# Performance work log

Measured on AMD Instinct MI355X. Metric: run time of the kernel, lower is better.

## Reference

```python
import jax, jax.numpy as jnp
import numpy as np

B, S, D, H = 4, 2048, 1024, 16
HS = D // H          # head size 64
DF = 4 * D           # ffn hidden 4096
EPS = 1e-5


def _layer_norm(x, g, b):
    mu = jnp.mean(x, axis=-1, keepdims=True)
    var = jnp.var(x, axis=-1, keepdims=True)
    return (x - mu) * jax.lax.rsqrt(var + EPS) * g + b


def setup_inputs() -> dict:
    key = jax.random.key(0)
    ks = jax.random.split(key, 12)
    s_d = 1.0 / np.sqrt(D)
    s_f = 1.0 / np.sqrt(DF)
    return {
        "x": jax.random.normal(ks[0], (B, S, D), jnp.float32),
        # per-head q/k/v projections, batched over heads: [H, D, HS]
        "wq": jax.random.uniform(ks[1], (H, D, HS), jnp.float32, -s_d, s_d),
        "wk": jax.random.uniform(ks[2], (H, D, HS), jnp.float32, -s_d, s_d),
        "wv": jax.random.uniform(ks[3], (H, D, HS), jnp.float32, -s_d, s_d),
        "proj_w": jax.random.uniform(ks[4], (D, D), jnp.float32, -s_d, s_d),
        "proj_b": jax.random.uniform(ks[5], (D,), jnp.float32, -s_d, s_d),
        "ff1_w": jax.random.uniform(ks[6], (D, DF), jnp.float32, -s_d, s_d),
        "ff1_b": jax.random.uniform(ks[7], (DF,), jnp.float32, -s_d, s_d),
        "ff2_w": jax.random.uniform(ks[8], (DF, D), jnp.float32, -s_f, s_f),
        "ff2_b": jax.random.uniform(ks[9], (D,), jnp.float32, -s_f, s_f),
        "ln1_g": jnp.ones((D,), jnp.float32),
        "ln1_b": jnp.zeros((D,), jnp.float32),
        "ln2_g": jnp.ones((D,), jnp.float32),
        "ln2_b": jnp.zeros((D,), jnp.float32),
    }


def reference(x, wq, wk, wv, proj_w, proj_b, ff1_w, ff1_b, ff2_w, ff2_b,
              ln1_g, ln1_b, ln2_g, ln2_b):
    # --- multi-head causal self-attention on ln1(x), all heads batched ---
    h = _layer_norm(x, ln1_g, ln1_b)                      # [B,S,D]
    q = jnp.einsum("bsd,hde->bhse", h, wq)                # [B,H,S,HS]
    k = jnp.einsum("bsd,hde->bhse", h, wk)
    v = jnp.einsum("bsd,hde->bhse", h, wv)
    scale = HS ** -0.5
    scores = jnp.einsum("bhse,bhte->bhst", q, k) * scale  # [B,H,S,S]
    causal = jnp.tril(jnp.ones((S, S), bool))
    scores = jnp.where(causal, scores, jnp.finfo(scores.dtype).min)
    att = jax.nn.softmax(scores, axis=-1)
    o = jnp.einsum("bhst,bhte->bhse", att, v)             # [B,H,S,HS]
    o = o.transpose(0, 2, 1, 3).reshape(B, S, D)          # concat heads
    sa = o @ proj_w + proj_b
    x = x + sa
    # --- FFN on ln2(x) ---
    h2 = _layer_norm(x, ln2_g, ln2_b)
    ff = jax.nn.relu(h2 @ ff1_w + ff1_b) @ ff2_w + ff2_b
    return x + ff
```

## Files before the change

kernel.cpp:

```cpp
#include <hip/hip_runtime.h>
#include <hip/hip_bf16.h>

#define BB 4
#define SS 2048
#define DD 1024
#define HH 16
#define HSZ 64
#define DFF 4096

typedef short short8 __attribute__((ext_vector_type(8)));
typedef float f32x4 __attribute__((ext_vector_type(4)));
typedef unsigned short us4 __attribute__((ext_vector_type(4)));

#define AS1 __attribute__((address_space(1)))
#define AS3 __attribute__((address_space(3)))

__device__ __forceinline__ unsigned short f2bf(float f) {
    return __bfloat16_as_ushort(__float2bfloat16(f));
}

__global__ __launch_bounds__(256) void pack_qkv_kernel(
    const float* __restrict__ wq, const float* __restrict__ wk,
    const float* __restrict__ wv, __hip_bfloat16* __restrict__ out)
{
    __shared__ float tile[64][65];
    const int bid = blockIdx.x;
    const int kt = bid & 15, hh = (bid >> 4) & 15, sel = bid >> 8;
    const float* src = (sel == 0) ? wq : (sel == 1) ? wk : wv;
    src += (size_t)hh * (DD * HSZ) + (size_t)kt * 64 * HSZ;
    const int tx = threadIdx.x & 63, ty = threadIdx.x >> 6;
    #pragma unroll
    for (int r = 0; r < 64; r += 4)
        tile[r + ty][tx] = src[(size_t)(r + ty) * HSZ + tx];
    __syncthreads();
    unsigned short* o = (unsigned short*)out + (size_t)(sel * DD + hh * 64) * DD + kt * 64;
    #pragma unroll
    for (int r = 0; r < 64; r += 4) {
        int e = r + ty;
        o[(size_t)e * DD + tx] = f2bf(tile[tx][e]);
    }
}

__global__ __launch_bounds__(256) void pack_T_kernel(
    const float* __restrict__ in, __hip_bfloat16* __restrict__ out, int K, int N)
{
    __shared__ float tile[64][65];
    const int nb = N >> 6;
    const int tn0 = (blockIdx.x % nb) << 6, tk0 = (blockIdx.x / nb) << 6;
    const int tx = threadIdx.x & 63, ty = threadIdx.x >> 6;
    #pragma unroll
    for (int r = 0; r < 64; r += 4)
        tile[r + ty][tx] = in[(size_t)(tk0 + r + ty) * N + tn0 + tx];
    __syncthreads();
    unsigned short* o = (unsigned short*)out;
    #pragma unroll
    for (int r = 0; r < 64; r += 4) {
        int n = r + ty;
        o[(size_t)(tn0 + n) * K + tk0 + tx] = f2bf(tile[tx][n]);
    }
}

__global__ __launch_bounds__(256) void ln_kernel(
    const float* __restrict__ x, const float* __restrict__ g,
    const float* __restrict__ b, __hip_bfloat16* __restrict__ out)
{
    int row = blockIdx.x;
    int t = threadIdx.x;
    const float4* xr = (const float4*)(x + (size_t)row * DD);
    float4 v = xr[t];
    float s = v.x + v.y + v.z + v.w;
    float ss = v.x * v.x + v.y * v.y + v.z * v.z + v.w * v.w;
    #pragma unroll
    for (int off = 32; off; off >>= 1) {
        s += __shfl_xor(s, off, 64);
        ss += __shfl_xor(ss, off, 64);
    }
    __shared__ float red[8];
    int w = t >> 6, lane = t & 63;
    if (lane == 0) { red[w] = s; red[4 + w] = ss; }
    __syncthreads();
    s = red[0] + red[1] + red[2] + red[3];
    ss = red[4] + red[5] + red[6] + red[7];
    float mu = s * (1.f / DD);
    float var = ss * (1.f / DD) - mu * mu;
    float rs = rsqrtf(var + 1e-5f);
    float4 gv = ((const float4*)g)[t];
    float4 bv = ((const float4*)b)[t];
    ushort4 pk = make_ushort4(
        f2bf((v.x - mu) * rs * gv.x + bv.x),
        f2bf((v.y - mu) * rs * gv.y + bv.y),
        f2bf((v.z - mu) * rs * gv.z + bv.z),
        f2bf((v.w - mu) * rs * gv.w + bv.w));
    *(ushort4*)((unsigned short*)out + (size_t)row * DD + t * 4) = pk;
}

template<int BN, bool BIAS, bool RELU, bool RES, bool OUTF32>
__global__ __launch_bounds__(512) void gemm_kernel(
    const __hip_bfloat16* __restrict__ A, const __hip_bfloat16* __restrict__ BT,
    const float* __restrict__ bias, const float* __restrict__ res,
    void* __restrict__ Cout, int M, int N, int K, int nbx)
{
    constexpr int NB = BN / 128;
    constexpr int NREP = BN / 64;
    __shared__ uint4 Ah[2][2][1024];
    __shared__ uint4 Bh[2][NB][1024];

    const int tid = threadIdx.x;
    const int lane = tid & 63;
    const int w = tid >> 6;
    const int lr = lane & 15, g = lane >> 4;
    const int nwg = gridDim.x;
    const int cpx = nwg >> 3;
    const int wg = blockIdx.x;
    const int swz = (wg & 7) * cpx + (wg >> 3);
    const int bx = swz % nbx, by = swz / nbx;
    const int row0 = by * 256, col0 = bx * BN;
    const int wm = w >> 2, wn = w & 3;
    const int NT = K >> 6;

    f32x4 acc0[4][NREP] = {};
    f32x4 acc1[4][NREP] = {};
    short8 bfr[NREP][2];

    auto stageA = [&](int buf, int half, int t) {
        const int k0 = t * 64;
        #pragma unroll
        for (int j = 0; j < 2; ++j) {
            int s = j * 512 + tid;
            int r = s >> 3;
            int c = (s & 7) ^ (r & 7);
            const __hip_bfloat16* src = A + (size_t)(row0 + half * 128 + r) * K + k0 + c * 8;
            __builtin_amdgcn_global_load_lds((const AS1 void*)src,
                (AS3 void*)(&Ah[buf][half][j * 512 + (tid & ~63)]), 16, 0, 0);
        }
    };
    auto stageB = [&](int buf, int half, int t) {
        const int k0 = t * 64;
        #pragma unroll
        for (int j = 0; j < 2; ++j) {
            int s = j * 512 + tid;
            int r = s >> 3;
            int c = (s & 7) ^ (r & 7);
            const __hip_bfloat16* src = BT + (size_t)(col0 + half * 128 + r) * K + k0 + c * 8;
            __builtin_amdgcn_global_load_lds((const AS1 void*)src,
                (AS3 void*)(&Bh[buf][half][j * 512 + (tid & ~63)]), 16, 0, 0);
        }
    };
    auto loadB = [&](int buf) {
        const int hb = (NB == 2) ? (wn >> 1) : 0;
        const int cb = (NB == 2) ? ((wn & 1) * 64) : (wn * 32);
        #pragma unroll
        for (int n = 0; n < NREP; ++n) {
            int c = cb + n * 16 + lr;
            #pragma unroll
            for (int kk = 0; kk < 2; ++kk)
                bfr[n][kk] = *(const short8*)&Bh[buf][hb][c * 8 + ((kk * 4 + g) ^ (c & 7))];
        }
    };
    auto phase = [&](auto& acc, int buf, int mh) {
        short8 af[4][2];
        #pragma unroll
        for (int mi = 0; mi < 4; ++mi) {
            int r = wm * 64 + mi * 16 + lr;
            #pragma unroll
            for (int kk = 0; kk < 2; ++kk)
                af[mi][kk] = *(const short8*)&Ah[buf][mh][r * 8 + ((kk * 4 + g) ^ (r & 7))];
        }
        asm volatile("s_waitcnt lgkmcnt(0)" ::: "memory");
        __builtin_amdgcn_sched_barrier(0);
        __builtin_amdgcn_s_setprio(1);
        #pragma unroll
        for (int mi = 0; mi < 4; ++mi)
            #pragma unroll
            for (int n = 0; n < NREP; ++n)
                #pragma unroll
                for (int kk = 0; kk < 2; ++kk)
                    acc[mi][n] = __builtin_amdgcn_mfma_f32_16x16x32_bf16(
                        af[mi][kk], bfr[n][kk], acc[mi][n], 0, 0, 0);
        __builtin_amdgcn_s_setprio(0);
    };

    stageA(0, 0, 0);
    stageB(0, 0, 0);
    if constexpr (NB == 2) stageB(0, 1, 0);
    stageA(0, 1, 0);
    stageA(1, 0, 1);
    if constexpr (NB == 2) stageB(1, 0, 1);

    for (int t = 0; t < NT; ++t) {
        const int buf = t & 1;
        if (t < NT - 1) {
            if constexpr (NB == 2) asm volatile("s_waitcnt vmcnt(4)" ::: "memory");
            else                   asm volatile("s_waitcnt vmcnt(2)" ::: "memory");
        } else {
            asm volatile("s_waitcnt vmcnt(0)" ::: "memory");
        }
        __builtin_amdgcn_s_barrier();
        __builtin_amdgcn_sched_barrier(0);
        if (t + 1 < NT) {
            if constexpr (NB == 2) { stageB(buf ^ 1, 1, t + 1); stageA(buf ^ 1, 1, t + 1); }
            else                   { stageB(buf ^ 1, 0, t + 1); stageA(buf ^ 1, 1, t + 1); }
        }
        loadB(buf);
        phase(acc0, buf, 0);
        if (t < NT - 1) {
            if constexpr (NB == 2) asm volatile("s_waitcnt vmcnt(8)" ::: "memory");
            else                   asm volatile("s_waitcnt vmcnt(6)" ::: "memory");
        } else {
            asm volatile("s_waitcnt vmcnt(0)" ::: "memory");
        }
        __builtin_amdgcn_s_barrier();
        __builtin_amdgcn_sched_barrier(0);
        if (t + 2 < NT) {
            stageA(buf, 0, t + 2);
            if constexpr (NB == 2) stageB(buf, 0, t + 2);
        }
        phase(acc1, buf, 1);
    }

    auto store = [&](auto& acc, int mh) {
        #pragma unroll
        for (int mi = 0; mi < 4; ++mi) {
            #pragma unroll
            for (int j = 0; j < 4; ++j) {
                int rr = row0 + mh * 128 + wm * 64 + mi * 16 + g * 4 + j;
                #pragma unroll
                for (int n = 0; n < NREP; ++n) {
                    int cc = col0 + wn * (NREP * 16) + n * 16 + lr;
                    float vv = acc[mi][n][j];
                    if (BIAS) vv += bias[cc];
                    if (RELU) vv = fmaxf(vv, 0.f);
                    if (RES) vv += res[(size_t)rr * N + cc];
                    if (OUTF32) ((float*)Cout)[(size_t)rr * N + cc] = vv;
                    else ((__hip_bfloat16*)Cout)[(size_t)rr * N + cc] = __float2bfloat16(vv);
                }
            }
        }
    };
    store(acc0, 0);
    store(acc1, 1);
}

__device__ __forceinline__ void stage_kv(
    const unsigned short* __restrict__ qkvu, size_t rowbase, int h, int kv0, int tl,
    unsigned short* __restrict__ Kb, unsigned short* __restrict__ Vb)
{
    {
        int kv = tl >> 2, c = tl & 3;
        const unsigned short* src = qkvu + rowbase + (size_t)(kv0 + kv) * 3072 + DD + h * HSZ + c * 16;
        uint4 v0 = *(const uint4*)src;
        uint4 v1 = *(const uint4*)(src + 8);
        int sw = kv & 7;
        *(uint4*)&Kb[kv * 64 + ((2 * c) ^ sw) * 8] = v0;
        *(uint4*)&Kb[kv * 64 + ((2 * c + 1) ^ sw) * 8] = v1;
    }
    {
        int bkv = ((tl >> 6) << 2) | (tl & 3);
        int bd = (tl >> 2) & 15;
        const unsigned short* src = qkvu + rowbase + (size_t)(kv0 + bkv * 4) * 3072 + 2 * DD + h * HSZ + bd * 4;
        us4 r0 = *(const us4*)src;
        us4 r1 = *(const us4*)(src + 3072);
        us4 r2 = *(const us4*)(src + 2 * 3072);
        us4 r3 = *(const us4*)(src + 3 * 3072);
        #pragma unroll
        for (int cc = 0; cc < 4; ++cc) {
            int d = bd * 4 + cc;
            us4 wv = { r0[cc], r1[cc], r2[cc], r3[cc] };
            *(us4*)&Vb[d * 64 + (((bkv >> 1) ^ (d & 7)) * 8) + (bkv & 1) * 4] = wv;
        }
    }
}

__device__ __forceinline__ void flash_tile(
    const unsigned short* __restrict__ Kb, const unsigned short* __restrict__ Vb,
    unsigned short* __restrict__ Pw, const short8* qfc, int qgc, int kv0, int q, int g,
    float& m_run, float& l_run, f32x4* oacc)
{
    f32x4 st[4] = {};
    __builtin_amdgcn_s_setprio(1);
    #pragma unroll
    for (int tt = 0; tt < 4; ++tt) {
        #pragma unroll
        for (int kk = 0; kk < 2; ++kk) {
            short8 kf = *(const short8*)&Kb[(tt * 16 + q) * 64 + ((4 * kk + g) ^ (q & 7)) * 8];
            st[tt] = __builtin_amdgcn_mfma_f32_16x16x32_bf16(kf, qfc[kk], st[tt], 0, 0, 0);
        }
    }
    __builtin_amdgcn_s_setprio(0);

    float mt = -1e30f;
    #pragma unroll
    for (int tt = 0; tt < 4; ++tt)
        #pragma unroll
        for (int j = 0; j < 4; ++j) {
            float s = st[tt][j] * 0.125f;
            int kvg = kv0 + tt * 16 + g * 4 + j;
            s = (kvg <= qgc) ? s : -1e30f;
            st[tt][j] = s;
            mt = fmaxf(mt, s);
        }
    mt = fmaxf(mt, __shfl_xor(mt, 16, 64));
    mt = fmaxf(mt, __shfl_xor(mt, 32, 64));
    float m_new = fmaxf(m_run, mt);
    float corr = __expf(m_run - m_new);
    float lsum = 0.f;
    #pragma unroll
    for (int tt = 0; tt < 4; ++tt)
        #pragma unroll
        for (int j = 0; j < 4; ++j) {
            float p = __expf(st[tt][j] - m_new);
            st[tt][j] = p;
            lsum += p;
        }
    lsum += __shfl_xor(lsum, 16, 64);
    lsum += __shfl_xor(lsum, 32, 64);
    l_run = l_run * corr + lsum;
    m_run = m_new;

    #pragma unroll
    for (int tt = 0; tt < 4; ++tt) {
        unsigned int lo = ((unsigned int)f2bf(st[tt][1]) << 16) | (unsigned int)f2bf(st[tt][0]);
        unsigned int hi = ((unsigned int)f2bf(st[tt][3]) << 16) | (unsigned int)f2bf(st[tt][2]);
        uint2 pk = make_uint2(lo, hi);
        *(uint2*)&Pw[q * 64 + ((2 * tt + (g >> 1)) ^ (q & 7)) * 8 + (g & 1) * 4] = pk;
    }

    #pragma unroll
    for (int j = 0; j < 4; ++j) {
        float cj = __shfl(corr, g * 4 + j, 64);
        #pragma unroll
        for (int dn = 0; dn < 4; ++dn)
            oacc[dn][j] *= cj;
    }

    __builtin_amdgcn_s_setprio(1);
    #pragma unroll
    for (int kk = 0; kk < 2; ++kk) {
        short8 pf = *(const short8*)&Pw[q * 64 + ((4 * kk + g) ^ (q & 7)) * 8];
        #pragma unroll
        for (int dn = 0; dn < 4; ++dn) {
            short8 vf = *(const short8*)&Vb[(dn * 16 + q) * 64 + ((4 * kk + g) ^ (q & 7)) * 8];
            oacc[dn] = __builtin_amdgcn_mfma_f32_16x16x32_bf16(pf, vf, oacc[dn], 0, 0, 0);
        }
    }
    __builtin_amdgcn_s_setprio(0);
}

__global__ __launch_bounds__(512) void attn_kernel(
    const __hip_bfloat16* __restrict__ qkv, __hip_bfloat16* __restrict__ o)
{
    __shared__ unsigned short K_lds[2][64 * 64];
    __shared__ unsigned short Vt_lds[2][64 * 64];
    __shared__ unsigned short P_lds[8 * 1024];

    const int t = threadIdx.x;
    const int lane = t & 63, w = t >> 6;
    const int grp = w >> 2, wq4 = w & 3, tl = t & 255;
    const int q = lane & 15, g = lane >> 4;
    const int pq = blockIdx.x & 15;
    const int h = (blockIdx.x >> 4) & 15;
    const int b = blockIdx.x >> 8;
    const int qtA = pq, qtB = 31 - pq;
    const int qt1 = grp ? qtB : qtA;
    const unsigned short* qkvu = (const unsigned short*)qkv;
    const size_t rowbase = (size_t)(b * SS) * 3072;
    unsigned short* Kb = K_lds[grp];
    unsigned short* Vb = Vt_lds[grp];
    unsigned short* Pw = &P_lds[w * 1024];
    unsigned short* op = (unsigned short*)o;

    int qgc = qt1 * 64 + wq4 * 16 + q;
    short8 qfc[2];
    #pragma unroll
    for (int kk = 0; kk < 2; ++kk)
        qfc[kk] = *(const short8*)(qkvu + rowbase + (size_t)qgc * 3072 + h * HSZ + kk * 32 + g * 8);

    f32x4 oacc[4] = {};
    float m_run = -1e30f, l_run = 0.f;

    for (int it = 0; it <= pq; ++it) {
        __syncthreads();
        stage_kv(qkvu, rowbase, h, it * 64, tl, Kb, Vb);
        __syncthreads();
        flash_tile(Kb, Vb, Pw, qfc, qgc, it * 64, q, g, m_run, l_run, oacc);
    }

    if (grp == 0) {
        #pragma unroll
        for (int j = 0; j < 4; ++j) {
            float lj = __shfl(l_run, g * 4 + j, 64);
            float inv = 1.f / lj;
            int orow = qtA * 64 + wq4 * 16 + g * 4 + j;
            #pragma unroll
            for (int dn = 0; dn < 4; ++dn)
                op[(size_t)(b * SS + orow) * DD + h * HSZ + dn * 16 + q] = f2bf(oacc[dn][j] * inv);
        }
        qgc = qtB * 64 + wq4 * 16 + q;
        #pragma unroll
        for (int kk = 0; kk < 2; ++kk)
            qfc[kk] = *(const short8*)(qkvu + rowbase + (size_t)qgc * 3072 + h * HSZ + kk * 32 + g * 8);
        m_run = -1e30f; l_run = 0.f;
        #pragma unroll
        for (int dn = 0; dn < 4; ++dn) oacc[dn] = f32x4{0.f, 0.f, 0.f, 0.f};
    }

    for (int it2 = 0; it2 < 16 - pq; ++it2) {
        int tile = grp ? (pq + 1 + it2) : (16 + it2);
        bool active = grp ? (tile <= 15) : true;
        __syncthreads();
        if (active) stage_kv(qkvu, rowbase, h, tile * 64, tl, Kb, Vb);
        __syncthreads();
        if (active) flash_tile(Kb, Vb, Pw, qfc, qgc, tile * 64, q, g, m_run, l_run, oacc);
    }

    __syncthreads();
    float* obuf = (float*)K_lds;
    float* mlbuf = (float*)P_lds;
    if (grp == 0) {
        #pragma unroll
        for (int dn = 0; dn < 4; ++dn)
            #pragma unroll
            for (int j = 0; j < 4; ++j)
                obuf[wq4 * 1024 + lane * 16 + dn * 4 + j] = oacc[dn][j];
        if (g == 0) { mlbuf[wq4 * 32 + q] = m_run; mlbuf[wq4 * 32 + 16 + q] = l_run; }
    }
    __syncthreads();
    if (grp == 1) {
        float mA = mlbuf[wq4 * 32 + q];
        float lA = mlbuf[wq4 * 32 + 16 + q];
        float mM = fmaxf(m_run, mA);
        float sB = __expf(m_run - mM);
        float sA = __expf(mA - mM);
        float lM = l_run * sB + lA * sA;
        #pragma unroll
        for (int j = 0; j < 4; ++j) {
            float sBj = __shfl(sB, g * 4 + j, 64);
            float sAj = __shfl(sA, g * 4 + j, 64);
            float lMj = __shfl(lM, g * 4 + j, 64);
            float inv = 1.f / lMj;
            int orow = qtB * 64 + wq4 * 16 + g * 4 + j;
            #pragma unroll
            for (int dn = 0; dn < 4; ++dn) {
                float oA = obuf[wq4 * 1024 + lane * 16 + dn * 4 + j];
                float vv = (oacc[dn][j] * sBj + oA * sAj) * inv;
                op[(size_t)(b * SS + orow) * DD + h * HSZ + dn * 16 + q] = f2bf(vv);
            }
        }
    }
}

extern "C" void kernel_launch(void* const* d_in, const int* in_sizes, int n_in,
                              void* d_out, int out_size, void* d_ws, size_t ws_size,
                              hipStream_t stream)
{
    const float* x      = (const float*)d_in[0];
    const float* wq     = (const float*)d_in[1];
    const float* wk     = (const float*)d_in[2];
    const float* wv     = (const float*)d_in[3];
    const float* proj_w = (const float*)d_in[4];
    const float* proj_b = (const float*)d_in[5];
    const float* ff1_w  = (const float*)d_in[6];
    const float* ff1_b  = (const float*)d_in[7];
    const float* ff2_w  = (const float*)d_in[8];
    const float* ff2_b  = (const float*)d_in[9];
    const float* ln1_g  = (const float*)d_in[10];
    const float* ln1_b  = (const float*)d_in[11];
    const float* ln2_g  = (const float*)d_in[12];
    const float* ln2_b  = (const float*)d_in[13];
    float* out = (float*)d_out;

    char* ws = (char*)d_ws;
    const size_t MB = 1ull << 20;
    __hip_bfloat16* h     = (__hip_bfloat16*)(ws);
    __hip_bfloat16* qkv   = (__hip_bfloat16*)(ws + 16 * MB);
    __hip_bfloat16* obuf  = (__hip_bfloat16*)(ws + 64 * MB);
    float*          x1    = (float*)(ws + 80 * MB);
    __hip_bfloat16* wqkvT = (__hip_bfloat16*)(ws + 112 * MB);
    __hip_bfloat16* projT = (__hip_bfloat16*)(ws + 118 * MB);
    __hip_bfloat16* ff1T  = (__hip_bfloat16*)(ws + 120 * MB);
    __hip_bfloat16* ff2T  = (__hip_bfloat16*)(ws + 128 * MB);
    __hip_bfloat16* f1    = (__hip_bfloat16*)(ws + 16 * MB);

    const int ROWS = BB * SS;

    pack_qkv_kernel<<<768, 256, 0, stream>>>(wq, wk, wv, wqkvT);
    pack_T_kernel<<<(DD / 64) * (DD / 64), 256, 0, stream>>>(proj_w, projT, DD, DD);
    pack_T_kernel<<<(DFF / 64) * (DD / 64), 256, 0, stream>>>(ff1_w, ff1T, DD, DFF);
    pack_T_kernel<<<(DD / 64) * (DFF / 64), 256, 0, stream>>>(ff2_w, ff2T, DFF, DD);

    ln_kernel<<<ROWS, 256, 0, stream>>>(x, ln1_g, ln1_b, h);
    gemm_kernel<128, false, false, false, false><<<(ROWS / 256) * (3 * DD / 128), 512, 0, stream>>>(
        h, wqkvT, nullptr, nullptr, qkv, ROWS, 3 * DD, DD, 3 * DD / 128);
    attn_kernel<<<BB * HH * 16, 512, 0, stream>>>(qkv, obuf);
    gemm_kernel<128, true, false, true, true><<<(ROWS / 256) * (DD / 128), 512, 0, stream>>>(
        obuf, projT, proj_b, x, x1, ROWS, DD, DD, DD / 128);
    ln_kernel<<<ROWS, 256, 0, stream>>>(x1, ln2_g, ln2_b, h);
    gemm_kernel<256, true, true, false, false><<<(ROWS / 256) * (DFF / 256), 512, 0, stream>>>(
        h, ff1T, ff1_b, nullptr, f1, ROWS, DFF, DD, DFF / 256);
    gemm_kernel<128, true, false, true, true><<<(ROWS / 256) * (DD / 128), 512, 0, stream>>>(
        f1, ff2T, ff2_b, x1, out, ROWS, DD, DFF, DD / 128);
}
```

Baseline: 418.3 us.

## Prefetch K/V tiles into registers and lazily rescale online softmax

The two phase loops of the attention kernel are merged into one 17-iteration loop. The next K/V tile's global loads are issued into registers before computing the current tile, then written to LDS after a barrier, so global latency overlaps with MFMA work. The causal mask is now applied only on the diagonal tile. Softmax uses exp2 with the 1/sqrt(d)·log2e scale folded in, and the running-max rescale of the accumulator is skipped when the new max stays within a threshold. This trades extra registers and a wave-wide vote for less global stall and less ALU work per tile.

Result: slower. 448.5 us (+7.2%).

```diff
diff --git a/kernel.cpp b/kernel.cpp
--- a/kernel.cpp
+++ b/kernel.cpp
@@ -241,40 +241,10 @@
     store(acc1, 1);
 }
 
-__device__ __forceinline__ void stage_kv(
-    const unsigned short* __restrict__ qkvu, size_t rowbase, int h, int kv0, int tl,
-    unsigned short* __restrict__ Kb, unsigned short* __restrict__ Vb)
-{
-    {
-        int kv = tl >> 2, c = tl & 3;
-        const unsigned short* src = qkvu + rowbase + (size_t)(kv0 + kv) * 3072 + DD + h * HSZ + c * 16;
-        uint4 v0 = *(const uint4*)src;
-        uint4 v1 = *(const uint4*)(src + 8);
-        int sw = kv & 7;
-        *(uint4*)&Kb[kv * 64 + ((2 * c) ^ sw) * 8] = v0;
-        *(uint4*)&Kb[kv * 64 + ((2 * c + 1) ^ sw) * 8] = v1;
-    }
-    {
-        int bkv = ((tl >> 6) << 2) | (tl & 3);
-        int bd = (tl >> 2) & 15;
-        const unsigned short* src = qkvu + rowbase + (size_t)(kv0 + bkv * 4) * 3072 + 2 * DD + h * HSZ + bd * 4;
-        us4 r0 = *(const us4*)src;
-        us4 r1 = *(const us4*)(src + 3072);
-        us4 r2 = *(const us4*)(src + 2 * 3072);
-        us4 r3 = *(const us4*)(src + 3 * 3072);
-        #pragma unroll
-        for (int cc = 0; cc < 4; ++cc) {
-            int d = bd * 4 + cc;
-            us4 wv = { r0[cc], r1[cc], r2[cc], r3[cc] };
-            *(us4*)&Vb[d * 64 + (((bkv >> 1) ^ (d & 7)) * 8) + (bkv & 1) * 4] = wv;
-        }
-    }
-}
-
 __device__ __forceinline__ void flash_tile(
     const unsigned short* __restrict__ Kb, const unsigned short* __restrict__ Vb,
     unsigned short* __restrict__ Pw, const short8* qfc, int qgc, int kv0, int q, int g,
-    float& m_run, float& l_run, f32x4* oacc)
+    float& m_run, float& l_run, f32x4* oacc, bool masked)
 {
     f32x4 st[4] = {};
     __builtin_amdgcn_s_setprio(1);
@@ -288,34 +258,59 @@
     }
     __builtin_amdgcn_s_setprio(0);
 
+    const float SC = 0.1803368801111731f;
     float mt = -1e30f;
-    #pragma unroll
-    for (int tt = 0; tt < 4; ++tt)
-        #pragma unroll
-        for (int j = 0; j < 4; ++j) {
-            float s = st[tt][j] * 0.125f;
-            int kvg = kv0 + tt * 16 + g * 4 + j;
-            s = (kvg <= qgc) ? s : -1e30f;
-            st[tt][j] = s;
-            mt = fmaxf(mt, s);
-        }
+    if (masked) {
+        #pragma unroll
+        for (int tt = 0; tt < 4; ++tt)
+            #pragma unroll
+            for (int j = 0; j < 4; ++j) {
+                float s = st[tt][j] * SC;
+                int kvg = kv0 + tt * 16 + g * 4 + j;
+                s = (kvg <= qgc) ? s : -1e30f;
+                st[tt][j] = s;
+                mt = fmaxf(mt, s);
+            }
+    } else {
+        #pragma unroll
+        for (int tt = 0; tt < 4; ++tt)
+            #pragma unroll
+            for (int j = 0; j < 4; ++j) {
+                float s = st[tt][j] * SC;
+                st[tt][j] = s;
+                mt = fmaxf(mt, s);
+            }
+    }
     mt = fmaxf(mt, __shfl_xor(mt, 16, 64));
     mt = fmaxf(mt, __shfl_xor(mt, 32, 64));
-    float m_new = fmaxf(m_run, mt);
-    float corr = __expf(m_run - m_new);
+
+    bool defer = __all(mt <= m_run + 11.0f);
+    if (!defer) {
+        float m_new = fmaxf(m_run, mt);
+        float corr = exp2f(m_run - m_new);
+        #pragma unroll
+        for (int j = 0; j < 4; ++j) {
+            float cj = __shfl(corr, g * 4 + j, 64);
+            #pragma unroll
+            for (int dn = 0; dn < 4; ++dn)
+                oacc[dn][j] *= cj;
+        }
+        l_run *= corr;
+        m_run = m_new;
+    }
+
     float lsum = 0.f;
     #pragma unroll
     for (int tt = 0; tt < 4; ++tt)
         #pragma unroll
         for (int j = 0; j < 4; ++j) {
-            float p = __expf(st[tt][j] - m_new);
+            float p = exp2f(st[tt][j] - m_run);
             st[tt][j] = p;
             lsum += p;
         }
     lsum += __shfl_xor(lsum, 16, 64);
     lsum += __shfl_xor(lsum, 32, 64);
-    l_run = l_run * corr + lsum;
-    m_run = m_new;
+    l_run += lsum;
 
     #pragma unroll
     for (int tt = 0; tt < 4; ++tt) {
@@ -323,14 +318,6 @@
         unsigned int hi = ((unsigned int)f2bf(st[tt][3]) << 16) | (unsigned int)f2bf(st[tt][2]);
         uint2 pk = make_uint2(lo, hi);
         *(uint2*)&Pw[q * 64 + ((2 * tt + (g >> 1)) ^ (q & 7)) * 8 + (g & 1) * 4] = pk;
-    }
-
-    #pragma unroll
-    for (int j = 0; j < 4; ++j) {
-        float cj = __shfl(corr, g * 4 + j, 64);
-        #pragma unroll
-        for (int dn = 0; dn < 4; ++dn)
-            oacc[dn][j] *= cj;
     }
 
     __builtin_amdgcn_s_setprio(1);
@@ -361,7 +348,6 @@
     const int h = (blockIdx.x >> 4) & 15;
     const int b = blockIdx.x >> 8;
     const int qtA = pq, qtB = 31 - pq;
-    const int qt1 = grp ? qtB : qtA;
     const unsigned short* qkvu = (const unsigned short*)qkv;
     const size_t rowbase = (size_t)(b * SS) * 3072;
     unsigned short* Kb = K_lds[grp];
@@ -369,7 +355,8 @@
     unsigned short* Pw = &P_lds[w * 1024];
     unsigned short* op = (unsigned short*)o;
 
-    int qgc = qt1 * 64 + wq4 * 16 + q;
+    int qt_cur = grp ? qtB : qtA;
+    int qgc = qt_cur * 64 + wq4 * 16 + q;
     short8 qfc[2];
     #pragma unroll
     for (int kk = 0; kk < 2; ++kk)
@@ -378,42 +365,73 @@
     f32x4 oacc[4] = {};
     float m_run = -1e30f, l_run = 0.f;
 
-    for (int it = 0; it <= pq; ++it) {
+    uint4 pk0, pk1;
+    us4 pv0, pv1, pv2, pv3;
+    const int s_kv = tl >> 2, s_c = tl & 3, s_sw = s_kv & 7;
+    const int s_bkv = ((tl >> 6) << 2) | (tl & 3);
+    const int s_bd = (tl >> 2) & 15;
+
+    auto load_regs = [&](int tile) {
+        int kv0 = tile * 64;
+        const unsigned short* ksrc = qkvu + rowbase + (size_t)(kv0 + s_kv) * 3072 + DD + h * HSZ + s_c * 16;
+        pk0 = *(const uint4*)ksrc;
+        pk1 = *(const uint4*)(ksrc + 8);
+        const unsigned short* vsrc = qkvu + rowbase + (size_t)(kv0 + s_bkv * 4) * 3072 + 2 * DD + h * HSZ + s_bd * 4;
+        pv0 = *(const us4*)vsrc;
+        pv1 = *(const us4*)(vsrc + 3072);
+        pv2 = *(const us4*)(vsrc + 2 * 3072);
+        pv3 = *(const us4*)(vsrc + 3 * 3072);
+    };
+    auto write_lds = [&]() {
+        *(uint4*)&Kb[s_kv * 64 + ((2 * s_c) ^ s_sw) * 8] = pk0;
+        *(uint4*)&Kb[s_kv * 64 + ((2 * s_c + 1) ^ s_sw) * 8] = pk1;
+        #pragma unroll
+        for (int cc = 0; cc < 4; ++cc) {
+            int d = s_bd * 4 + cc;
+            us4 wv = { pv0[cc], pv1[cc], pv2[cc], pv3[cc] };
+            *(us4*)&Vb[d * 64 + (((s_bkv >> 1) ^ (d & 7)) * 8) + (s_bkv & 1) * 4] = wv;
+        }
+    };
+    auto tile_of = [&](int it) { return grp ? it : (it <= pq ? it : it + 15 - pq); };
+    auto active_of = [&](int it) { return grp ? (it <= 15) : true; };
+
+    load_regs(tile_of(0));
+    write_lds();
+    __syncthreads();
+
+    for (int it = 0; it < 17; ++it) {
+        const bool act = active_of(it);
+        const bool nact = (it + 1 < 17) && active_of(it + 1);
+        if (nact) load_regs(tile_of(it + 1));
+        if (act) {
+            int tile = tile_of(it);
+            flash_tile(Kb, Vb, Pw, qfc, qgc, tile * 64, q, g, m_run, l_run, oacc,
+                       tile == qt_cur);
+        }
+        if (grp == 0 && it == pq) {
+            #pragma unroll
+            for (int j = 0; j < 4; ++j) {
+                float lj = __shfl(l_run, g * 4 + j, 64);
+                float inv = 1.f / lj;
+                int orow = qtA * 64 + wq4 * 16 + g * 4 + j;
+                #pragma unroll
+                for (int dn = 0; dn < 4; ++dn)
+                    op[(size_t)(b * SS + orow) * DD + h * HSZ + dn * 16 + q] = f2bf(oacc[dn][j] * inv);
+            }
+            qt_cur = qtB;
+            qgc = qtB * 64 + wq4 * 16 + q;
+            #pragma unroll
+            for (int kk = 0; kk < 2; ++kk)
+                qfc[kk] = *(const short8*)(qkvu + rowbase + (size_t)qgc * 3072 + h * HSZ + kk * 32 + g * 8);
+            m_run = -1e30f; l_run = 0.f;
+            #pragma unroll
+            for (int dn = 0; dn < 4; ++dn) oacc[dn] = f32x4{0.f, 0.f, 0.f, 0.f};
+        }
         __syncthreads();
-        stage_kv(qkvu, rowbase, h, it * 64, tl, Kb, Vb);
+        if (nact) write_lds();
         __syncthreads();
-        flash_tile(Kb, Vb, Pw, qfc, qgc, it * 64, q, g, m_run, l_run, oacc);
-    }
-
-    if (grp == 0) {
-        #pragma unroll
-        for (int j = 0; j < 4; ++j) {
-            float lj = __shfl(l_run, g * 4 + j, 64);
-            float inv = 1.f / lj;
-            int orow = qtA * 64 + wq4 * 16 + g * 4 + j;
-            #pragma unroll
-            for (int dn = 0; dn < 4; ++dn)
-                op[(size_t)(b * SS + orow) * DD + h * HSZ + dn * 16 + q] = f2bf(oacc[dn][j] * inv);
-        }
-        qgc = qtB * 64 + wq4 * 16 + q;
-        #pragma unroll
-        for (int kk = 0; kk < 2; ++kk)
-            qfc[kk] = *(const short8*)(qkvu + rowbase + (size_t)qgc * 3072 + h * HSZ + kk * 32 + g * 8);
-        m_run = -1e30f; l_run = 0.f;
-        #pragma unroll
-        for (int dn = 0; dn < 4; ++dn) oacc[dn] = f32x4{0.f, 0.f, 0.f, 0.f};
-    }
-
-    for (int it2 = 0; it2 < 16 - pq; ++it2) {
-        int tile = grp ? (pq + 1 + it2) : (16 + it2);
-        bool active = grp ? (tile <= 15) : true;
-        __syncthreads();
-        if (active) stage_kv(qkvu, rowbase, h, tile * 64, tl, Kb, Vb);
-        __syncthreads();
-        if (active) flash_tile(Kb, Vb, Pw, qfc, qgc, tile * 64, q, g, m_run, l_run, oacc);
-    }
-
-    __syncthreads();
+    }
+
     float* obuf = (float*)K_lds;
     float* mlbuf = (float*)P_lds;
     if (grp == 0) {
@@ -429,8 +447,8 @@
         float mA = mlbuf[wq4 * 32 + q];
         float lA = mlbuf[wq4 * 32 + 16 + q];
         float mM = fmaxf(m_run, mA);
-        float sB = __expf(m_run - mM);
-        float sA = __expf(mA - mM);
+        float sB = exp2f(m_run - mM);
+        float sA = exp2f(mA - mM);
         float lM = l_run * sB + lA * sA;
         #pragma unroll
         for (int j = 0; j < 4; ++j) {
```

## Skip causal mask on full tiles, defer rescaling, use exp2, shrink P buffer

Applied to the files above, without the earlier changes.

Attention softmax now applies the causal mask only on the diagonal tile and folds the 1/sqrt(d)*log2(e) factor into one scale so exp2f can replace __expf. Rescaling of the output accumulator and running sum is skipped when no lane's tile max exceeds the running max by more than a threshold. P is written and read in half-tile chunks interleaved with the PV MFMAs, which halves the P LDS buffer, and launch bounds request higher occupancy. The aim is fewer ALU ops and less LDS per block. The cost is extra branching, and the deferred rescale relies on fp32 headroom for unnormalized exponentials.

Result: slower. 538.8 us (+28.8%).

```diff
diff --git a/kernel.cpp b/kernel.cpp
--- a/kernel.cpp
+++ b/kernel.cpp
@@ -274,7 +274,7 @@
 __device__ __forceinline__ void flash_tile(
     const unsigned short* __restrict__ Kb, const unsigned short* __restrict__ Vb,
     unsigned short* __restrict__ Pw, const short8* qfc, int qgc, int kv0, int q, int g,
-    float& m_run, float& l_run, f32x4* oacc)
+    float& m_run, float& l_run, f32x4* oacc, bool masked)
 {
     f32x4 st[4] = {};
     __builtin_amdgcn_s_setprio(1);
@@ -288,55 +288,72 @@
     }
     __builtin_amdgcn_s_setprio(0);
 
+    const float SC = 0.1803368801111731f;
     float mt = -1e30f;
-    #pragma unroll
-    for (int tt = 0; tt < 4; ++tt)
-        #pragma unroll
-        for (int j = 0; j < 4; ++j) {
-            float s = st[tt][j] * 0.125f;
-            int kvg = kv0 + tt * 16 + g * 4 + j;
-            s = (kvg <= qgc) ? s : -1e30f;
-            st[tt][j] = s;
-            mt = fmaxf(mt, s);
-        }
+    if (masked) {
+        #pragma unroll
+        for (int tt = 0; tt < 4; ++tt)
+            #pragma unroll
+            for (int j = 0; j < 4; ++j) {
+                float s = st[tt][j] * SC;
+                int kvg = kv0 + tt * 16 + g * 4 + j;
+                s = (kvg <= qgc) ? s : -1e30f;
+                st[tt][j] = s;
+                mt = fmaxf(mt, s);
+            }
+    } else {
+        #pragma unroll
+        for (int tt = 0; tt < 4; ++tt)
+            #pragma unroll
+            for (int j = 0; j < 4; ++j) {
+                float s = st[tt][j] * SC;
+                st[tt][j] = s;
+                mt = fmaxf(mt, s);
+            }
+    }
     mt = fmaxf(mt, __shfl_xor(mt, 16, 64));
     mt = fmaxf(mt, __shfl_xor(mt, 32, 64));
-    float m_new = fmaxf(m_run, mt);
-    float corr = __expf(m_run - m_new);
+
+    bool defer = __all(mt <= m_run + 11.0f);
+    if (!defer) {
+        float m_new = fmaxf(m_run, mt);
+        float corr = exp2f(m_run - m_new);
+        #pragma unroll
+        for (int j = 0; j < 4; ++j) {
+            float cj = __shfl(corr, g * 4 + j, 64);
+            #pragma unroll
+            for (int dn = 0; dn < 4; ++dn)
+                oacc[dn][j] *= cj;
+        }
+        l_run *= corr;
+        m_run = m_new;
+    }
+
     float lsum = 0.f;
     #pragma unroll
     for (int tt = 0; tt < 4; ++tt)
         #pragma unroll
         for (int j = 0; j < 4; ++j) {
-            float p = __expf(st[tt][j] - m_new);
+            float p = exp2f(st[tt][j] - m_run);
             st[tt][j] = p;
             lsum += p;
         }
     lsum += __shfl_xor(lsum, 16, 64);
     lsum += __shfl_xor(lsum, 32, 64);
-    l_run = l_run * corr + lsum;
-    m_run = m_new;
-
-    #pragma unroll
-    for (int tt = 0; tt < 4; ++tt) {
-        unsigned int lo = ((unsigned int)f2bf(st[tt][1]) << 16) | (unsigned int)f2bf(st[tt][0]);
-        unsigned int hi = ((unsigned int)f2bf(st[tt][3]) << 16) | (unsigned int)f2bf(st[tt][2]);
-        uint2 pk = make_uint2(lo, hi);
-        *(uint2*)&Pw[q * 64 + ((2 * tt + (g >> 1)) ^ (q & 7)) * 8 + (g & 1) * 4] = pk;
-    }
-
-    #pragma unroll
-    for (int j = 0; j < 4; ++j) {
-        float cj = __shfl(corr, g * 4 + j, 64);
-        #pragma unroll
-        for (int dn = 0; dn < 4; ++dn)
-            oacc[dn][j] *= cj;
-    }
+    l_run += lsum;
 
     __builtin_amdgcn_s_setprio(1);
     #pragma unroll
     for (int kk = 0; kk < 2; ++kk) {
-        short8 pf = *(const short8*)&Pw[q * 64 + ((4 * kk + g) ^ (q & 7)) * 8];
+        #pragma unroll
+        for (int rt = 0; rt < 2; ++rt) {
+            int tt = kk * 2 + rt;
+            unsigned int lo = ((unsigned int)f2bf(st[tt][1]) << 16) | (unsigned int)f2bf(st[tt][0]);
+            unsigned int hi = ((unsigned int)f2bf(st[tt][3]) << 16) | (unsigned int)f2bf(st[tt][2]);
+            uint2 pk = make_uint2(lo, hi);
+            *(uint2*)&Pw[q * 32 + ((2 * rt + (g >> 1)) ^ ((q >> 1) & 3)) * 8 + (g & 1) * 4] = pk;
+        }
+        short8 pf = *(const short8*)&Pw[q * 32 + (g ^ ((q >> 1) & 3)) * 8];
         #pragma unroll
         for (int dn = 0; dn < 4; ++dn) {
             short8 vf = *(const short8*)&Vb[(dn * 16 + q) * 64 + ((4 * kk + g) ^ (q & 7)) * 8];
@@ -346,12 +363,12 @@
     __builtin_amdgcn_s_setprio(0);
 }
 
-__global__ __launch_bounds__(512) void attn_kernel(
+__global__ __launch_bounds__(512, 8) void attn_kernel(
     const __hip_bfloat16* __restrict__ qkv, __hip_bfloat16* __restrict__ o)
 {
     __shared__ unsigned short K_lds[2][64 * 64];
     __shared__ unsigned short Vt_lds[2][64 * 64];
-    __shared__ unsigned short P_lds[8 * 1024];
+    __shared__ unsigned short P_lds[8 * 512];
 
     const int t = threadIdx.x;
     const int lane = t & 63, w = t >> 6;
@@ -366,10 +383,11 @@
     const size_t rowbase = (size_t)(b * SS) * 3072;
     unsigned short* Kb = K_lds[grp];
     unsigned short* Vb = Vt_lds[grp];
-    unsigned short* Pw = &P_lds[w * 1024];
+    unsigned short* Pw = &P_lds[w * 512];
     unsigned short* op = (unsigned short*)o;
 
-    int qgc = qt1 * 64 + wq4 * 16 + q;
+    int qt_cur = qt1;
+    int qgc = qt_cur * 64 + wq4 * 16 + q;
     short8 qfc[2];
     #pragma unroll
     for (int kk = 0; kk < 2; ++kk)
@@ -382,7 +400,7 @@
         __syncthreads();
         stage_kv(qkvu, rowbase, h, it * 64, tl, Kb, Vb);
         __syncthreads();
-        flash_tile(Kb, Vb, Pw, qfc, qgc, it * 64, q, g, m_run, l_run, oacc);
+        flash_tile(Kb, Vb, Pw, qfc, qgc, it * 64, q, g, m_run, l_run, oacc, it == qt_cur);
     }
 
     if (grp == 0) {
@@ -395,6 +413,7 @@
             for (int dn = 0; dn < 4; ++dn)
                 op[(size_t)(b * SS + orow) * DD + h * HSZ + dn * 16 + q] = f2bf(oacc[dn][j] * inv);
         }
+        qt_cur = qtB;
         qgc = qtB * 64 + wq4 * 16 + q;
         #pragma unroll
         for (int kk = 0; kk < 2; ++kk)
@@ -410,7 +429,8 @@
         __syncthreads();
         if (active) stage_kv(qkvu, rowbase, h, tile * 64, tl, Kb, Vb);
         __syncthreads();
-        if (active) flash_tile(Kb, Vb, Pw, qfc, qgc, tile * 64, q, g, m_run, l_run, oacc);
+        if (active) flash_tile(Kb, Vb, Pw, qfc, qgc, tile * 64, q, g, m_run, l_run, oacc,
+                               tile == qt_cur);
     }
 
     __syncthreads();
@@ -429,8 +449,8 @@
         float mA = mlbuf[wq4 * 32 + q];
         float lA = mlbuf[wq4 * 32 + 16 + q];
         float mM = fmaxf(m_run, mA);
-        float sB = __expf(m_run - mM);
-        float sA = __expf(mA - mM);
+        float sB = exp2f(m_run - mM);
+        float sA = exp2f(mA - mM);
         float lM = l_run * sB + lA * sA;
         #pragma unroll
         for (int j = 0; j < 4; ++j) {
```
